# Kernel tuning notes

Measured on AMD Instinct MI355X. Metric: run time of the kernel, lower is better.

## Reference

```python
import jax, jax.numpy as jnp
import numpy as np

N_POS = 8192          # number of positive samples
N_NEG = 4000          # negatives per positive
N_TOT = N_POS + N_POS * N_NEG


def setup_inputs() -> dict:
    key = jax.random.key(0)
    k1, k2 = jax.random.split(key)
    predict_val = jax.random.normal(k1, (N_TOT,), dtype=jnp.float32)
    # 'index' is a permutation; the module reorders predict_val by argsort(index)
    index = jax.random.permutation(k2, jnp.arange(N_TOT, dtype=jnp.int64))
    return {"predict_val": predict_val, "index": index, "num": N_NEG, "num_pos": N_POS}


def reference(predict_val, index, num, num_pos):
    # index_tuple = sorted(enumerate(index)) by value -> reorder by argsort(index)
    pv = predict_val[jnp.argsort(index)]
    pos = pv[:num_pos]                                  # [num_pos]
    neg = pv[num_pos:num_pos + num_pos * num]
    neg = neg.reshape(num_pos, num)                     # [num_pos, num]
    # rank of pos among {neg, pos} sorted descending == 1 + #(neg > pos)
    # (ties are randomly broken in the original; measure-zero for continuous scores)
    rank = 1 + jnp.sum(neg > pos[:, None], axis=-1)     # [num_pos], int
    sample_mrr = 1.0 / rank.astype(pv.dtype)            # [num_pos]
    mrr = jnp.mean(sample_mrr)
    return mrr, sample_mrr
```

## Files before the change

kernel.cpp:

```cpp
#include <hip/hip_runtime.h>


constexpr int N_POS = 8192;
constexpr int N_NEG = 4000;
constexpr int CNT_BLOCKS = 512;
constexpr int NSLOT = N_POS / 4;

typedef int   vint4   __attribute__((ext_vector_type(4)));
typedef float vfloat4 __attribute__((ext_vector_type(4)));
typedef unsigned int  u32;
typedef unsigned long long u64;

__global__ __launch_bounds__(256) void scatter_pos_kernel(
    const vint4* __restrict__ idx4, const float* __restrict__ pv,
    float* __restrict__ pos, int nvec) {
  const int stride = gridDim.x * blockDim.x;
  int j = blockIdx.x * blockDim.x + threadIdx.x;
#define SC_ELEM(V, JJ)                                   \
  if ((V).x < N_POS) pos[(V).x] = pv[4 * (JJ) + 0];      \
  if ((V).y < N_POS) pos[(V).y] = pv[4 * (JJ) + 1];      \
  if ((V).z < N_POS) pos[(V).z] = pv[4 * (JJ) + 2];      \
  if ((V).w < N_POS) pos[(V).w] = pv[4 * (JJ) + 3];
  for (; j + stride < nvec; j += 2 * stride) {
    vint4 a = __builtin_nontemporal_load(&idx4[j]);
    vint4 b = __builtin_nontemporal_load(&idx4[j + stride]);
    SC_ELEM(a, j)
    SC_ELEM(b, j + stride)
  }
  for (; j < nvec; j += stride) {
    vint4 a = __builtin_nontemporal_load(&idx4[j]);
    SC_ELEM(a, j)
  }
#undef SC_ELEM
}

__global__ __launch_bounds__(1024) void count_kernel(
    const vint4* __restrict__ idx4, const vfloat4* __restrict__ pv4,
    const float* __restrict__ pos, u64* __restrict__ slab, int nvec) {
  __shared__ float pos_lds[N_POS];
  __shared__ u32 lcnt[N_POS];
  for (int i = threadIdx.x; i < N_POS; i += 1024) {
    pos_lds[i] = pos[i];
    lcnt[i] = 0u;
  }
  __syncthreads();

  const int stride = gridDim.x * blockDim.x;
  int j = blockIdx.x * blockDim.x + threadIdx.x;
#define CT_ELEM(IV, XV)                                              \
  if ((IV) >= N_POS) {                                               \
    unsigned r = (unsigned)((IV) - N_POS) / (unsigned)N_NEG;         \
    if ((XV) > pos_lds[r]) atomicAdd(&lcnt[r], 1u);                  \
  }
#define CT_VEC(V, X)                                                 \
  CT_ELEM((V).x, (X).x) CT_ELEM((V).y, (X).y)                        \
  CT_ELEM((V).z, (X).z) CT_ELEM((V).w, (X).w)
  for (; j + stride < nvec; j += 2 * stride) {
    vint4 va = __builtin_nontemporal_load(&idx4[j]);
    vint4 vb = __builtin_nontemporal_load(&idx4[j + stride]);
    vfloat4 xa = __builtin_nontemporal_load(&pv4[j]);
    vfloat4 xb = __builtin_nontemporal_load(&pv4[j + stride]);
    CT_VEC(va, xa)
    CT_VEC(vb, xb)
  }
  for (; j < nvec; j += stride) {
    vint4 va = __builtin_nontemporal_load(&idx4[j]);
    vfloat4 xa = __builtin_nontemporal_load(&pv4[j]);
    CT_VEC(va, xa)
  }
#undef CT_VEC
#undef CT_ELEM
  __syncthreads();

  u64* my = slab + (size_t)blockIdx.x * NSLOT;
  const uint4* lq = (const uint4*)lcnt;
  for (int s = threadIdx.x; s < NSLOT; s += 1024) {
    uint4 q = lq[s];
    u64 p = (u64)(q.x & 0xFFFFu) | ((u64)(q.y & 0xFFFFu) << 16) |
            ((u64)(q.z & 0xFFFFu) << 32) | ((u64)(q.w & 0xFFFFu) << 48);
    __builtin_nontemporal_store(p, &my[s]);
  }
}

__global__ __launch_bounds__(1024) void reduce_kernel(
    const u64* __restrict__ slab, float* __restrict__ out) {
  int k = blockIdx.x * 1024 + threadIdx.x;
  int slot = k >> 3, part = k & 7;
  u64 acc = 0;
  const u64* base = slab + (size_t)(part * 64) * NSLOT + slot;
#pragma unroll 8
  for (int b = 0; b < 64; ++b) acc += base[(size_t)b * NSLOT];
  acc += __shfl_down(acc, 4, 64);
  acc += __shfl_down(acc, 2, 64);
  acc += __shfl_down(acc, 1, 64);

  float lsum = 0.f;
  if (part == 0) {
    float m0 = 1.0f / (float)(1u + (u32)(acc & 0xFFFFu));
    float m1 = 1.0f / (float)(1u + (u32)((acc >> 16) & 0xFFFFu));
    float m2 = 1.0f / (float)(1u + (u32)((acc >> 32) & 0xFFFFu));
    float m3 = 1.0f / (float)(1u + (u32)((acc >> 48) & 0xFFFFu));
    vfloat4 m = {m0, m1, m2, m3};
    *(vfloat4*)&out[1 + 4 * slot] = m;
    lsum = m0 + m1 + m2 + m3;
  }
  __shared__ float wsum[16];
#pragma unroll
  for (int off = 32; off > 0; off >>= 1) lsum += __shfl_down(lsum, off, 64);
  int t = threadIdx.x;
  if ((t & 63) == 0) wsum[t >> 6] = lsum;
  __syncthreads();
  if (t < 64) {
    float v = (t < 16) ? wsum[t] : 0.f;
#pragma unroll
    for (int off = 8; off > 0; off >>= 1) v += __shfl_down(v, off, 64);
    if (t == 0) atomicAdd(&out[0], v / (float)N_POS);
  }
}

extern "C" void kernel_launch(void* const* d_in, const int* in_sizes, int n_in,
                              void* d_out, int out_size, void* d_ws, size_t ws_size,
                              hipStream_t stream) {
  const float* pv = (const float*)d_in[0];
  const int* idx = (const int*)d_in[1];
  float* out = (float*)d_out;

  float* pos = (float*)d_ws;
  u64* slab = (u64*)((char*)d_ws + 32 * 1024);

  int n = in_sizes[0];
  int nvec = n / 4;

  hipMemsetAsync(out, 0, sizeof(float), stream);
  scatter_pos_kernel<<<2048, 256, 0, stream>>>((const vint4*)idx, pv, pos, nvec);
  count_kernel<<<CNT_BLOCKS, 1024, 0, stream>>>((const vint4*)idx,
                                                (const vfloat4*)pv, pos, slab,
                                                nvec);
  reduce_kernel<<<16, 1024, 0, stream>>>(slab, out);
}
```

Measured before the change: 309.2 us.

## Fuse scatter, count and reduce into one cooperative kernel with grid syncs

```diff
diff --git a/kernel.cpp b/kernel.cpp
--- a/kernel.cpp
+++ b/kernel.cpp
@@ -1,140 +1,135 @@
 #include <hip/hip_runtime.h>
+#include <hip/hip_cooperative_groups.h>
+
+namespace cg = cooperative_groups;
 
 
 constexpr int N_POS = 8192;
 constexpr int N_NEG = 4000;
-constexpr int CNT_BLOCKS = 512;
+constexpr int BLOCKS = 512;
+constexpr int THREADS = 512;
 constexpr int NSLOT = N_POS / 4;
 
 typedef int   vint4   __attribute__((ext_vector_type(4)));
 typedef float vfloat4 __attribute__((ext_vector_type(4)));
-typedef unsigned int  u32;
+typedef unsigned int u32;
 typedef unsigned long long u64;
 
-__global__ __launch_bounds__(256) void scatter_pos_kernel(
+__global__ __launch_bounds__(THREADS, 4) void mrr_fused(
     const vint4* __restrict__ idx4, const float* __restrict__ pv,
-    float* __restrict__ pos, int nvec) {
-  const int stride = gridDim.x * blockDim.x;
-  int j = blockIdx.x * blockDim.x + threadIdx.x;
+    float* __restrict__ pos, u64* __restrict__ cnt, float* __restrict__ out,
+    int nvec) {
+  __shared__ float pos_lds[N_POS];
+  __shared__ u32   lcnt[N_POS];
+  __shared__ float wsum[THREADS / 64];
+
+  cg::grid_group grid = cg::this_grid();
+  const int gtid = blockIdx.x * THREADS + threadIdx.x;
+  const int stride = BLOCKS * THREADS;
+
+  if (gtid < NSLOT) cnt[gtid] = 0ull;
+  {
+    int j = gtid;
 #define SC_ELEM(V, JJ)                                   \
-  if ((V).x < N_POS) pos[(V).x] = pv[4 * (JJ) + 0];      \
-  if ((V).y < N_POS) pos[(V).y] = pv[4 * (JJ) + 1];      \
-  if ((V).z < N_POS) pos[(V).z] = pv[4 * (JJ) + 2];      \
-  if ((V).w < N_POS) pos[(V).w] = pv[4 * (JJ) + 3];
-  for (; j + stride < nvec; j += 2 * stride) {
-    vint4 a = __builtin_nontemporal_load(&idx4[j]);
-    vint4 b = __builtin_nontemporal_load(&idx4[j + stride]);
-    SC_ELEM(a, j)
-    SC_ELEM(b, j + stride)
+    if ((V).x < N_POS) pos[(V).x] = pv[4 * (JJ) + 0];    \
+    if ((V).y < N_POS) pos[(V).y] = pv[4 * (JJ) + 1];    \
+    if ((V).z < N_POS) pos[(V).z] = pv[4 * (JJ) + 2];    \
+    if ((V).w < N_POS) pos[(V).w] = pv[4 * (JJ) + 3];
+    for (; j + stride < nvec; j += 2 * stride) {
+      vint4 a = __builtin_nontemporal_load(&idx4[j]);
+      vint4 b = __builtin_nontemporal_load(&idx4[j + stride]);
+      SC_ELEM(a, j)
+      SC_ELEM(b, j + stride)
+    }
+    for (; j < nvec; j += stride) {
+      vint4 a = __builtin_nontemporal_load(&idx4[j]);
+      SC_ELEM(a, j)
+    }
+#undef SC_ELEM
   }
-  for (; j < nvec; j += stride) {
-    vint4 a = __builtin_nontemporal_load(&idx4[j]);
-    SC_ELEM(a, j)
-  }
-#undef SC_ELEM
-}
+  grid.sync();
 
-__global__ __launch_bounds__(1024) void count_kernel(
-    const vint4* __restrict__ idx4, const vfloat4* __restrict__ pv4,
-    const float* __restrict__ pos, u64* __restrict__ slab, int nvec) {
-  __shared__ float pos_lds[N_POS];
-  __shared__ u32 lcnt[N_POS];
-  for (int i = threadIdx.x; i < N_POS; i += 1024) {
+  for (int i = threadIdx.x; i < N_POS; i += THREADS) {
     pos_lds[i] = pos[i];
     lcnt[i] = 0u;
   }
   __syncthreads();
 
-  const int stride = gridDim.x * blockDim.x;
-  int j = blockIdx.x * blockDim.x + threadIdx.x;
+  {
+    const vfloat4* __restrict__ pv4 = (const vfloat4*)pv;
+    int j = gtid;
 #define CT_ELEM(IV, XV)                                              \
-  if ((IV) >= N_POS) {                                               \
-    unsigned r = (unsigned)((IV) - N_POS) / (unsigned)N_NEG;         \
-    if ((XV) > pos_lds[r]) atomicAdd(&lcnt[r], 1u);                  \
-  }
+    if ((IV) >= N_POS) {                                             \
+      unsigned r = (unsigned)((IV) - N_POS) / (unsigned)N_NEG;       \
+      if ((XV) > pos_lds[r]) atomicAdd(&lcnt[r], 1u);                \
+    }
 #define CT_VEC(V, X)                                                 \
-  CT_ELEM((V).x, (X).x) CT_ELEM((V).y, (X).y)                        \
-  CT_ELEM((V).z, (X).z) CT_ELEM((V).w, (X).w)
-  for (; j + stride < nvec; j += 2 * stride) {
-    vint4 va = __builtin_nontemporal_load(&idx4[j]);
-    vint4 vb = __builtin_nontemporal_load(&idx4[j + stride]);
-    vfloat4 xa = __builtin_nontemporal_load(&pv4[j]);
-    vfloat4 xb = __builtin_nontemporal_load(&pv4[j + stride]);
-    CT_VEC(va, xa)
-    CT_VEC(vb, xb)
-  }
-  for (; j < nvec; j += stride) {
-    vint4 va = __builtin_nontemporal_load(&idx4[j]);
-    vfloat4 xa = __builtin_nontemporal_load(&pv4[j]);
-    CT_VEC(va, xa)
-  }
+    CT_ELEM((V).x, (X).x) CT_ELEM((V).y, (X).y)                      \
+    CT_ELEM((V).z, (X).z) CT_ELEM((V).w, (X).w)
+    for (; j + stride < nvec; j += 2 * stride) {
+      vint4 va = __builtin_nontemporal_load(&idx4[j]);
+      vint4 vb = __builtin_nontemporal_load(&idx4[j + stride]);
+      vfloat4 xa = __builtin_nontemporal_load(&pv4[j]);
+      vfloat4 xb = __builtin_nontemporal_load(&pv4[j + stride]);
+      CT_VEC(va, xa)
+      CT_VEC(vb, xb)
+    }
+    for (; j < nvec; j += stride) {
+      vint4 va = __builtin_nontemporal_load(&idx4[j]);
+      vfloat4 xa = __builtin_nontemporal_load(&pv4[j]);
+      CT_VEC(va, xa)
+    }
 #undef CT_VEC
 #undef CT_ELEM
+  }
   __syncthreads();
 
-  u64* my = slab + (size_t)blockIdx.x * NSLOT;
-  const uint4* lq = (const uint4*)lcnt;
-  for (int s = threadIdx.x; s < NSLOT; s += 1024) {
-    uint4 q = lq[s];
-    u64 p = (u64)(q.x & 0xFFFFu) | ((u64)(q.y & 0xFFFFu) << 16) |
-            ((u64)(q.z & 0xFFFFu) << 32) | ((u64)(q.w & 0xFFFFu) << 48);
-    __builtin_nontemporal_store(p, &my[s]);
+  for (int s = threadIdx.x; s < NSLOT; s += THREADS) {
+    u32 c0 = lcnt[4 * s + 0], c1 = lcnt[4 * s + 1];
+    u32 c2 = lcnt[4 * s + 2], c3 = lcnt[4 * s + 3];
+    u64 p = (u64)c0 | ((u64)c1 << 16) | ((u64)c2 << 32) | ((u64)c3 << 48);
+    if (p) atomicAdd(&cnt[s], p);
   }
-}
+  grid.sync();
 
-__global__ __launch_bounds__(1024) void reduce_kernel(
-    const u64* __restrict__ slab, float* __restrict__ out) {
-  int k = blockIdx.x * 1024 + threadIdx.x;
-  int slot = k >> 3, part = k & 7;
-  u64 acc = 0;
-  const u64* base = slab + (size_t)(part * 64) * NSLOT + slot;
-#pragma unroll 8
-  for (int b = 0; b < 64; ++b) acc += base[(size_t)b * NSLOT];
-  acc += __shfl_down(acc, 4, 64);
-  acc += __shfl_down(acc, 2, 64);
-  acc += __shfl_down(acc, 1, 64);
-
-  float lsum = 0.f;
-  if (part == 0) {
-    float m0 = 1.0f / (float)(1u + (u32)(acc & 0xFFFFu));
-    float m1 = 1.0f / (float)(1u + (u32)((acc >> 16) & 0xFFFFu));
-    float m2 = 1.0f / (float)(1u + (u32)((acc >> 32) & 0xFFFFu));
-    float m3 = 1.0f / (float)(1u + (u32)((acc >> 48) & 0xFFFFu));
-    vfloat4 m = {m0, m1, m2, m3};
-    *(vfloat4*)&out[1 + 4 * slot] = m;
-    lsum = m0 + m1 + m2 + m3;
-  }
-  __shared__ float wsum[16];
+  if (blockIdx.x == 0) {
+    float lsum = 0.f;
+    for (int s = threadIdx.x; s < NSLOT; s += THREADS) {
+      u64 p = __hip_atomic_load(&cnt[s], __ATOMIC_RELAXED,
+                                __HIP_MEMORY_SCOPE_AGENT);
 #pragma unroll
-  for (int off = 32; off > 0; off >>= 1) lsum += __shfl_down(lsum, off, 64);
-  int t = threadIdx.x;
-  if ((t & 63) == 0) wsum[t >> 6] = lsum;
-  __syncthreads();
-  if (t < 64) {
-    float v = (t < 16) ? wsum[t] : 0.f;
+      for (int e = 0; e < 4; ++e) {
+        u32 c = (u32)(p >> (16 * e)) & 0xFFFFu;
+        float m = 1.0f / (float)(1u + c);
+        out[1 + 4 * s + e] = m;
+        lsum += m;
+      }
+    }
 #pragma unroll
-    for (int off = 8; off > 0; off >>= 1) v += __shfl_down(v, off, 64);
-    if (t == 0) atomicAdd(&out[0], v / (float)N_POS);
+    for (int off = 32; off > 0; off >>= 1) lsum += __shfl_down(lsum, off, 64);
+    if ((threadIdx.x & 63) == 0) wsum[threadIdx.x >> 6] = lsum;
+    __syncthreads();
+    if (threadIdx.x == 0) {
+      float tot = 0.f;
+#pragma unroll
+      for (int w = 0; w < THREADS / 64; ++w) tot += wsum[w];
+      out[0] = tot / (float)N_POS;
+    }
   }
 }
 
 extern "C" void kernel_launch(void* const* d_in, const int* in_sizes, int n_in,
                               void* d_out, int out_size, void* d_ws, size_t ws_size,
                               hipStream_t stream) {
+  const vint4* idx4 = (const vint4*)d_in[1];
   const float* pv = (const float*)d_in[0];
-  const int* idx = (const int*)d_in[1];
   float* out = (float*)d_out;
+  float* pos = (float*)d_ws;
+  u64* cnt = (u64*)((char*)d_ws + 32 * 1024);
+  int nvec = in_sizes[0] / 4;
 
-  float* pos = (float*)d_ws;
-  u64* slab = (u64*)((char*)d_ws + 32 * 1024);
-
-  int n = in_sizes[0];
-  int nvec = n / 4;
-
-  hipMemsetAsync(out, 0, sizeof(float), stream);
-  scatter_pos_kernel<<<2048, 256, 0, stream>>>((const vint4*)idx, pv, pos, nvec);
-  count_kernel<<<CNT_BLOCKS, 1024, 0, stream>>>((const vint4*)idx,
-                                                (const vfloat4*)pv, pos, slab,
-                                                nvec);
-  reduce_kernel<<<16, 1024, 0, stream>>>(slab, out);
+  void* args[] = {(void*)&idx4, (void*)&pv, (void*)&pos,
+                  (void*)&cnt,  (void*)&out, (void*)&nvec};
+  hipLaunchCooperativeKernel((void*)mrr_fused, dim3(BLOCKS), dim3(THREADS),
+                             args, 0, stream);
 }
```

Measured after the change: 401.4 us. 1.3x slower.

## Use global atomics for counts, drop memset, cache index reads for reuse

Applied to the files above, without the earlier changes.

```diff
diff --git a/kernel.cpp b/kernel.cpp
--- a/kernel.cpp
+++ b/kernel.cpp
@@ -3,32 +3,33 @@
 
 constexpr int N_POS = 8192;
 constexpr int N_NEG = 4000;
-constexpr int CNT_BLOCKS = 512;
 constexpr int NSLOT = N_POS / 4;
 
 typedef int   vint4   __attribute__((ext_vector_type(4)));
 typedef float vfloat4 __attribute__((ext_vector_type(4)));
-typedef unsigned int  u32;
+typedef unsigned int u32;
 typedef unsigned long long u64;
 
 __global__ __launch_bounds__(256) void scatter_pos_kernel(
     const vint4* __restrict__ idx4, const float* __restrict__ pv,
-    float* __restrict__ pos, int nvec) {
-  const int stride = gridDim.x * blockDim.x;
-  int j = blockIdx.x * blockDim.x + threadIdx.x;
+    float* __restrict__ pos, u64* __restrict__ cnt, int nvec) {
+  const int gtid = blockIdx.x * 256 + threadIdx.x;
+  if (gtid < NSLOT) cnt[gtid] = 0ull;
+  const int stride = gridDim.x * 256;
+  int j = gtid;
 #define SC_ELEM(V, JJ)                                   \
   if ((V).x < N_POS) pos[(V).x] = pv[4 * (JJ) + 0];      \
   if ((V).y < N_POS) pos[(V).y] = pv[4 * (JJ) + 1];      \
   if ((V).z < N_POS) pos[(V).z] = pv[4 * (JJ) + 2];      \
   if ((V).w < N_POS) pos[(V).w] = pv[4 * (JJ) + 3];
   for (; j + stride < nvec; j += 2 * stride) {
-    vint4 a = __builtin_nontemporal_load(&idx4[j]);
-    vint4 b = __builtin_nontemporal_load(&idx4[j + stride]);
+    vint4 a = idx4[j];
+    vint4 b = idx4[j + stride];
     SC_ELEM(a, j)
     SC_ELEM(b, j + stride)
   }
   for (; j < nvec; j += stride) {
-    vint4 a = __builtin_nontemporal_load(&idx4[j]);
+    vint4 a = idx4[j];
     SC_ELEM(a, j)
   }
 #undef SC_ELEM
@@ -36,17 +37,17 @@
 
 __global__ __launch_bounds__(1024) void count_kernel(
     const vint4* __restrict__ idx4, const vfloat4* __restrict__ pv4,
-    const float* __restrict__ pos, u64* __restrict__ slab, int nvec) {
+    const float* __restrict__ pos, u64* __restrict__ cnt, int nvec) {
   __shared__ float pos_lds[N_POS];
-  __shared__ u32 lcnt[N_POS];
+  __shared__ u32   lcnt[N_POS];
   for (int i = threadIdx.x; i < N_POS; i += 1024) {
     pos_lds[i] = pos[i];
     lcnt[i] = 0u;
   }
   __syncthreads();
 
-  const int stride = gridDim.x * blockDim.x;
-  int j = blockIdx.x * blockDim.x + threadIdx.x;
+  const int stride = gridDim.x * 1024;
+  int j = blockIdx.x * 1024 + threadIdx.x;
 #define CT_ELEM(IV, XV)                                              \
   if ((IV) >= N_POS) {                                               \
     unsigned r = (unsigned)((IV) - N_POS) / (unsigned)N_NEG;         \
@@ -56,15 +57,15 @@
   CT_ELEM((V).x, (X).x) CT_ELEM((V).y, (X).y)                        \
   CT_ELEM((V).z, (X).z) CT_ELEM((V).w, (X).w)
   for (; j + stride < nvec; j += 2 * stride) {
-    vint4 va = __builtin_nontemporal_load(&idx4[j]);
-    vint4 vb = __builtin_nontemporal_load(&idx4[j + stride]);
+    vint4 va = idx4[j];
+    vint4 vb = idx4[j + stride];
     vfloat4 xa = __builtin_nontemporal_load(&pv4[j]);
     vfloat4 xb = __builtin_nontemporal_load(&pv4[j + stride]);
     CT_VEC(va, xa)
     CT_VEC(vb, xb)
   }
   for (; j < nvec; j += stride) {
-    vint4 va = __builtin_nontemporal_load(&idx4[j]);
+    vint4 va = idx4[j];
     vfloat4 xa = __builtin_nontemporal_load(&pv4[j]);
     CT_VEC(va, xa)
   }
@@ -72,49 +73,38 @@
 #undef CT_ELEM
   __syncthreads();
 
-  u64* my = slab + (size_t)blockIdx.x * NSLOT;
-  const uint4* lq = (const uint4*)lcnt;
   for (int s = threadIdx.x; s < NSLOT; s += 1024) {
-    uint4 q = lq[s];
-    u64 p = (u64)(q.x & 0xFFFFu) | ((u64)(q.y & 0xFFFFu) << 16) |
-            ((u64)(q.z & 0xFFFFu) << 32) | ((u64)(q.w & 0xFFFFu) << 48);
-    __builtin_nontemporal_store(p, &my[s]);
+    u32 c0 = lcnt[4 * s + 0], c1 = lcnt[4 * s + 1];
+    u32 c2 = lcnt[4 * s + 2], c3 = lcnt[4 * s + 3];
+    u64 p = (u64)c0 | ((u64)c1 << 16) | ((u64)c2 << 32) | ((u64)c3 << 48);
+    if (p) atomicAdd(&cnt[s], p);
   }
 }
 
-__global__ __launch_bounds__(1024) void reduce_kernel(
-    const u64* __restrict__ slab, float* __restrict__ out) {
-  int k = blockIdx.x * 1024 + threadIdx.x;
-  int slot = k >> 3, part = k & 7;
-  u64 acc = 0;
-  const u64* base = slab + (size_t)(part * 64) * NSLOT + slot;
-#pragma unroll 8
-  for (int b = 0; b < 64; ++b) acc += base[(size_t)b * NSLOT];
-  acc += __shfl_down(acc, 4, 64);
-  acc += __shfl_down(acc, 2, 64);
-  acc += __shfl_down(acc, 1, 64);
-
+__global__ __launch_bounds__(1024) void finalize_kernel(
+    const u64* __restrict__ cnt, float* __restrict__ out) {
+  __shared__ float wsum[16];
+  int t = threadIdx.x;
   float lsum = 0.f;
-  if (part == 0) {
-    float m0 = 1.0f / (float)(1u + (u32)(acc & 0xFFFFu));
-    float m1 = 1.0f / (float)(1u + (u32)((acc >> 16) & 0xFFFFu));
-    float m2 = 1.0f / (float)(1u + (u32)((acc >> 32) & 0xFFFFu));
-    float m3 = 1.0f / (float)(1u + (u32)((acc >> 48) & 0xFFFFu));
+  for (int s = t; s < NSLOT; s += 1024) {
+    u64 p = cnt[s];
+    float m0 = 1.0f / (float)(1u + (u32)(p & 0xFFFFu));
+    float m1 = 1.0f / (float)(1u + (u32)((p >> 16) & 0xFFFFu));
+    float m2 = 1.0f / (float)(1u + (u32)((p >> 32) & 0xFFFFu));
+    float m3 = 1.0f / (float)(1u + (u32)((p >> 48) & 0xFFFFu));
     vfloat4 m = {m0, m1, m2, m3};
-    *(vfloat4*)&out[1 + 4 * slot] = m;
-    lsum = m0 + m1 + m2 + m3;
+    *(vfloat4*)&out[1 + 4 * s] = m;
+    lsum += m0 + m1 + m2 + m3;
   }
-  __shared__ float wsum[16];
 #pragma unroll
   for (int off = 32; off > 0; off >>= 1) lsum += __shfl_down(lsum, off, 64);
-  int t = threadIdx.x;
   if ((t & 63) == 0) wsum[t >> 6] = lsum;
   __syncthreads();
-  if (t < 64) {
-    float v = (t < 16) ? wsum[t] : 0.f;
+  if (t == 0) {
+    float tot = 0.f;
 #pragma unroll
-    for (int off = 8; off > 0; off >>= 1) v += __shfl_down(v, off, 64);
-    if (t == 0) atomicAdd(&out[0], v / (float)N_POS);
+    for (int w = 0; w < 16; ++w) tot += wsum[w];
+    out[0] = tot / (float)N_POS;
   }
 }
 
@@ -124,17 +114,13 @@
   const float* pv = (const float*)d_in[0];
   const int* idx = (const int*)d_in[1];
   float* out = (float*)d_out;
+  float* pos = (float*)d_ws;
+  u64* cnt = (u64*)((char*)d_ws + 32 * 1024);
+  int nvec = in_sizes[0] / 4;
 
-  float* pos = (float*)d_ws;
-  u64* slab = (u64*)((char*)d_ws + 32 * 1024);
-
-  int n = in_sizes[0];
-  int nvec = n / 4;
-
-  hipMemsetAsync(out, 0, sizeof(float), stream);
-  scatter_pos_kernel<<<2048, 256, 0, stream>>>((const vint4*)idx, pv, pos, nvec);
-  count_kernel<<<CNT_BLOCKS, 1024, 0, stream>>>((const vint4*)idx,
-                                                (const vfloat4*)pv, pos, slab,
-                                                nvec);
-  reduce_kernel<<<16, 1024, 0, stream>>>(slab, out);
+  scatter_pos_kernel<<<2048, 256, 0, stream>>>((const vint4*)idx, pv, pos,
+                                               cnt, nvec);
+  count_kernel<<<512, 1024, 0, stream>>>((const vint4*)idx, (const vfloat4*)pv,
+                                         pos, cnt, nvec);
+  finalize_kernel<<<1, 1024, 0, stream>>>(cnt, out);
 }
```

New measurement: 289.1 us. 1.07x faster.
